# Performance work log

Hardware: AMD Instinct MI355X
Metric: run time of the kernel (lower is better)

## Reference

```python
import jax, jax.numpy as jnp
import numpy as np

WS = (7, 7, 7)          # (Wz, Wh, Ww)
NUM_HEADS = 3


def rel_position_index(ws):
    # Faithful to meshgrid_3d in the source: arrays are reversed, grid i varies
    # along axis i, so coords are stacked in (w, h, z) order.
    wz, wh, ww = ws
    g = np.meshgrid(np.arange(ww), np.arange(wh), np.arange(wz), indexing='ij')
    coords = np.stack(g)                      # (3, ww, wh, wz)
    flat = coords.reshape(3, -1)              # (3, N)
    rel = flat[:, :, None] - flat[:, None, :]  # (3, N, N)
    rel = rel.transpose(1, 2, 0).astype(np.int64)  # (N, N, 3)
    rel[:, :, 0] += wz - 1
    rel[:, :, 1] += wh - 1
    rel[:, :, 2] += ww - 1
    rel[:, :, 0] *= (2 * wh - 1) * (2 * ww - 1)
    rel[:, :, 1] *= (2 * ww - 1)
    return rel.sum(-1)                        # (N, N) in [0, (2W-1)^3)


REL_IDX = jnp.asarray(rel_position_index(WS).reshape(-1), dtype=jnp.int32)


def setup_inputs() -> dict:
    key = jax.random.key(0)
    ks = jax.random.split(key, 6)
    B, N, C = 256, 343, 96
    nW = 32
    x = jax.random.normal(ks[0], (B, N, C), dtype=jnp.float32)
    # shifted-window mask: 0 where attendable, -100 where blocked
    keep = jax.random.uniform(ks[1], (nW, N, N)) < 0.9
    mask = jnp.where(keep, 0.0, -100.0).astype(jnp.float32)
    w_qkv = jax.random.normal(ks[2], (C, 3 * C), dtype=jnp.float32) * 0.05
    b_qkv = jnp.zeros((3 * C,), jnp.float32)
    bias_table = jax.random.normal(ks[3], (2197, NUM_HEADS), dtype=jnp.float32) * 0.02
    w_proj = jax.random.normal(ks[4], (C, C), dtype=jnp.float32) * 0.05
    b_proj = jnp.zeros((C,), jnp.float32)
    return {"x": x, "mask": mask, "w_qkv": w_qkv, "b_qkv": b_qkv,
            "bias_table": bias_table, "w_proj": w_proj, "b_proj": b_proj}


def reference(x, mask, w_qkv, b_qkv, bias_table, w_proj, b_proj):
    B, N, C = x.shape
    H = NUM_HEADS
    hd = C // H
    scale = hd ** -0.5  # qk_scale is None -> head_dim**-0.5 (swin v1 path)
    # QKV projection, split to heads: (3, B, H, N, hd)
    qkv = (x @ w_qkv + b_qkv).reshape(B, N, 3, H, hd).transpose(2, 0, 3, 1, 4)
    q, k, v = qkv[0] * scale, qkv[1], qkv[2]
    attn = jnp.einsum('bhnd,bhmd->bhnm', q, k)        # (B, H, N, N)
    # gathered relative-position bias -> (H, N, N)
    bias = bias_table[REL_IDX].reshape(N, N, H).transpose(2, 0, 1)
    attn = attn + bias[None]
    # shifted-window mask add: reshape to (B//nW, nW, H, N, N)
    nW = mask.shape[0]
    attn = attn.reshape(B // nW, nW, H, N, N) + mask[None, :, None]
    attn = jax.nn.softmax(attn.reshape(B, H, N, N), axis=-1)
    out = jnp.einsum('bhnm,bhmd->bhnd', attn, v)      # (B, H, N, hd)
    out = out.transpose(0, 2, 1, 3).reshape(B, N, C)
    return out @ w_proj + b_proj
```

## Files before the change

kernel.cpp:

```cpp
#include <hip/hip_runtime.h>

#define N_TOK 343
#define NP 352
#define C_DIM 96
#define HEADS 3
#define HD 32
#define B_SZ 256
#define NW 32
#define QKV_COLS 288

#define QKV_ELEMS (B_SZ * HEADS * N_TOK * HD)
#define X2_ELEMS ((long)B_SZ * N_TOK * C_DIM)
#define CMB_ELEMS ((long)NW * HEADS * N_TOK * NP)

typedef _Float16 f16;
typedef _Float16 f16x2 __attribute__((ext_vector_type(2)));
typedef _Float16 f16x4 __attribute__((ext_vector_type(4)));
typedef _Float16 f16x8 __attribute__((ext_vector_type(8)));
typedef float f32x4 __attribute__((ext_vector_type(4)));

__global__ __launch_bounds__(256) void wprep_kernel(
    const float* __restrict__ w_qkv, const float* __restrict__ w_proj,
    f16* __restrict__ wt_qkv, f16* __restrict__ wt_proj) {
  const int e = blockIdx.x * 256 + threadIdx.x;
  if (e < QKV_COLS * 96) {
    const int cc = e / 96, k = e % 96;
    wt_qkv[e] = (f16)w_qkv[k * QKV_COLS + cc];
  } else {
    const int e2 = e - QKV_COLS * 96;
    if (e2 < 96 * 96) {
      const int cc = e2 / 96, k = e2 % 96;
      wt_proj[e2] = (f16)w_proj[k * 96 + cc];
    }
  }
}

__global__ __launch_bounds__(256) void cmb_kernel(
    const float* __restrict__ mask, const float* __restrict__ bias_table,
    f16* __restrict__ cmb) {
  const long e = (long)blockIdx.x * 256 + threadIdx.x;
  if (e >= CMB_ELEMS) return;
  const int key = (int)(e % NP);
  const long rowid = e / NP;
  const int q = (int)(rowid % N_TOK);
  const int wh = (int)(rowid / N_TOK);
  const int h = wh % HEADS;
  const int w = wh / HEADS;
  float val;
  if (key < N_TOK) {
    const int bn = (q / 49) * 169 + ((q / 7) % 7) * 13 + (q % 7);
    const int bm = (key / 49) * 169 + ((key / 7) % 7) * 13 + (key % 7);
    val = bias_table[(bn - bm + 1098) * HEADS + h] +
          mask[((long)w * N_TOK + q) * N_TOK + key];
  } else {
    val = -1000.f;
  }
  cmb[e] = (f16)val;
}

__global__ __launch_bounds__(256) void qkv_mfma_kernel(
    const float* __restrict__ x, const f16* __restrict__ wt,
    const float* __restrict__ bias,
    f16* __restrict__ Q, f16* __restrict__ K, f16* __restrict__ V) {
  __shared__ f16 sh[4][16][40];
  const int tid = threadIdx.x;
  const int wave = tid >> 6, lane = tid & 63;
  const int c = lane & 15, g = lane >> 4;
  const long rowTile = (long)blockIdx.x * 64 + wave * 16;
  const long arow = rowTile + c;

  f16x8 af[3];
#pragma unroll
  for (int ks = 0; ks < 3; ++ks) {
    const float* px = x + arow * 96 + ks * 32 + g * 8;
    const float4 lo = *(const float4*)px;
    const float4 hi = *(const float4*)(px + 4);
    f16x8 v;
    v[0] = (f16)lo.x; v[1] = (f16)lo.y; v[2] = (f16)lo.z; v[3] = (f16)lo.w;
    v[4] = (f16)hi.x; v[5] = (f16)hi.y; v[6] = (f16)hi.z; v[7] = (f16)hi.w;
    af[ks] = v;
  }

  const int rowL = (int)rowTile + (lane >> 2);
  const int bL = rowL / N_TOK, nL = rowL % N_TOK;

  const f32x4 zero = {0.f, 0.f, 0.f, 0.f};
  const float scale = 0.17677669529663687f;

#pragma unroll
  for (int p = 0; p < 9; ++p) {
    const int which = p / 3;
    const int h = p % 3;
    const float mult = (which == 0) ? scale : 1.0f;
#pragma unroll
    for (int e = 0; e < 2; ++e) {
      const int ct = 2 * p + e;
      f32x4 acc = zero;
#pragma unroll
      for (int ks = 0; ks < 3; ++ks) {
        const f16x8 bf = *(const f16x8*)(wt + (ct * 16 + c) * 96 + ks * 32 + g * 8);
        acc = __builtin_amdgcn_mfma_f32_16x16x32_f16(af[ks], bf, acc, 0, 0, 0);
      }
      const float bv = bias[ct * 16 + c];
#pragma unroll
      for (int r = 0; r < 4; ++r)
        sh[wave][4 * g + r][(e << 4) + c] = (f16)((acc[r] + bv) * mult);
    }
    __builtin_amdgcn_wave_barrier();
    const f16x8 po = *(const f16x8*)&sh[wave][lane >> 2][(lane & 3) * 8];
    __builtin_amdgcn_wave_barrier();
    f16* dst = (which == 0) ? Q : (which == 1) ? K : V;
    *(f16x8*)(dst + (((long)bL * HEADS + h) * N_TOK + nL) * HD + (lane & 3) * 8) = po;
  }
}

__global__ __launch_bounds__(512) void attn_kernel(
    const f16* __restrict__ Qh, const f16* __restrict__ Kh,
    const f16* __restrict__ Vh, const f16* __restrict__ CMB,
    f16* __restrict__ X2h) {
  __shared__ f16 Ks[NP][40];
  __shared__ f16 Vt[HD][356];

  const int blk = blockIdx.x;
  const int b = blk / HEADS;
  const int h = blk % HEADS;
  const int tid = threadIdx.x;
  const int wave = tid >> 6;
  const int lane = tid & 63;
  const int c = lane & 15;
  const int g = lane >> 4;

  const f16* Kg = Kh + (long)blk * (N_TOK * HD);
  const f16* Vg = Vh + (long)blk * (N_TOK * HD);
  const f16* Qg = Qh + (long)blk * (N_TOK * HD);

  for (int u = tid; u < NP * 4; u += 512) {
    const int key = u >> 2, j = u & 3;
    f16x8 val = {0, 0, 0, 0, 0, 0, 0, 0};
    if (key < N_TOK) val = *(const f16x8*)(Kg + key * HD + j * 8);
    *(f16x8*)&Ks[key][j * 8] = val;
  }
  for (int i = tid; i < N_TOK * 16; i += 512) {
    const int n = i >> 4, dp = i & 15;
    const f16x2 v2 = *(const f16x2*)(Vg + n * HD + dp * 2);
    Vt[2 * dp][n] = v2.x;
    Vt[2 * dp + 1][n] = v2.y;
  }
  for (int i = tid; i < HD * 13; i += 512) Vt[i / 13][N_TOK + i % 13] = (f16)0;
  __syncthreads();

  const int w = b & (NW - 1);
  const f32x4 zero = {0.f, 0.f, 0.f, 0.f};

  for (int qt = wave; qt < NP / 16; qt += 8) {
    const int q = qt * 16 + c;
    const int qrow = (q < N_TOK) ? q : (N_TOK - 1);
    const f16x8 qf = *(const f16x8*)(Qg + qrow * HD + g * 8);
    const f16* cmrow = CMB + ((long)(w * HEADS + h) * N_TOK + qrow) * NP;

    f32x4 acc0 = zero, acc1 = zero;
    float lsum = 0.f;

    for (int kt = 0; kt < NP / 32; ++kt) {
      const f16x8 kf0 = *(const f16x8*)&Ks[32 * kt + c][g * 8];
      const f16x8 kf1 = *(const f16x8*)&Ks[32 * kt + 16 + c][g * 8];
      const f16x4 cm0 = *(const f16x4*)(cmrow + 32 * kt + 4 * g);
      const f16x4 cm1 = *(const f16x4*)(cmrow + 32 * kt + 16 + 4 * g);

      const f32x4 s0 = __builtin_amdgcn_mfma_f32_16x16x32_f16(kf0, qf, zero, 0, 0, 0);
      const f32x4 s1 = __builtin_amdgcn_mfma_f32_16x16x32_f16(kf1, qf, zero, 0, 0, 0);

      float p0[4], p1[4];
#pragma unroll
      for (int r = 0; r < 4; ++r) {
        p0[r] = __expf(s0[r] + (float)cm0[r]);
        p1[r] = __expf(s1[r] + (float)cm1[r]);
        lsum += p0[r] + p1[r];
      }
      const f16x2 a0 = __builtin_bit_cast(f16x2, __builtin_amdgcn_cvt_pkrtz(p0[0], p0[1]));
      const f16x2 a1 = __builtin_bit_cast(f16x2, __builtin_amdgcn_cvt_pkrtz(p0[2], p0[3]));
      const f16x2 a2 = __builtin_bit_cast(f16x2, __builtin_amdgcn_cvt_pkrtz(p1[0], p1[1]));
      const f16x2 a3 = __builtin_bit_cast(f16x2, __builtin_amdgcn_cvt_pkrtz(p1[2], p1[3]));
      const f16x4 plo = __builtin_shufflevector(a0, a1, 0, 1, 2, 3);
      const f16x4 phi = __builtin_shufflevector(a2, a3, 0, 1, 2, 3);
      const f16x8 pf = __builtin_shufflevector(plo, phi, 0, 1, 2, 3, 4, 5, 6, 7);

      const f16x4 va0 = *(const f16x4*)&Vt[c][32 * kt + 4 * g];
      const f16x4 va1 = *(const f16x4*)&Vt[c][32 * kt + 16 + 4 * g];
      const f16x4 vb0 = *(const f16x4*)&Vt[16 + c][32 * kt + 4 * g];
      const f16x4 vb1 = *(const f16x4*)&Vt[16 + c][32 * kt + 16 + 4 * g];
      const f16x8 vf0 = __builtin_shufflevector(va0, va1, 0, 1, 2, 3, 4, 5, 6, 7);
      const f16x8 vf1 = __builtin_shufflevector(vb0, vb1, 0, 1, 2, 3, 4, 5, 6, 7);

      acc0 = __builtin_amdgcn_mfma_f32_16x16x32_f16(vf0, pf, acc0, 0, 0, 0);
      acc1 = __builtin_amdgcn_mfma_f32_16x16x32_f16(vf1, pf, acc1, 0, 0, 0);
    }

    lsum += __shfl_xor(lsum, 16);
    lsum += __shfl_xor(lsum, 32);
    const float inv = 1.f / lsum;

    if (q < N_TOK) {
      f16* orow = X2h + ((long)b * N_TOK + q) * C_DIM + h * HD;
      f16x4 o0, o1;
#pragma unroll
      for (int r = 0; r < 4; ++r) {
        o0[r] = (f16)(acc0[r] * inv);
        o1[r] = (f16)(acc1[r] * inv);
      }
      *(f16x4*)(orow + 4 * g) = o0;
      *(f16x4*)(orow + 16 + 4 * g) = o1;
    }
  }
}

__global__ __launch_bounds__(256) void proj_mfma_kernel(
    const f16* __restrict__ X2h, const f16* __restrict__ wt,
    const float* __restrict__ bias, float* __restrict__ out) {
  __shared__ float shp[4][16][100];
  const int tid = threadIdx.x;
  const int wave = tid >> 6, lane = tid & 63;
  const int c = lane & 15, g = lane >> 4;
  const long rowTile = (long)blockIdx.x * 64 + wave * 16;
  const long arow = rowTile + c;

  f16x8 af[3];
#pragma unroll
  for (int ks = 0; ks < 3; ++ks)
    af[ks] = *(const f16x8*)(X2h + arow * 96 + ks * 32 + g * 8);

  const f32x4 zero = {0.f, 0.f, 0.f, 0.f};
#pragma unroll
  for (int ct = 0; ct < 6; ++ct) {
    f32x4 acc = zero;
#pragma unroll
    for (int ks = 0; ks < 3; ++ks) {
      const f16x8 bf = *(const f16x8*)(wt + (ct * 16 + c) * 96 + ks * 32 + g * 8);
      acc = __builtin_amdgcn_mfma_f32_16x16x32_f16(af[ks], bf, acc, 0, 0, 0);
    }
    const float bv = bias[ct * 16 + c];
#pragma unroll
    for (int r = 0; r < 4; ++r)
      shp[wave][4 * g + r][ct * 16 + c] = acc[r] + bv;
  }
  __builtin_amdgcn_wave_barrier();
#pragma unroll
  for (int i = 0; i < 6; ++i) {
    const int u = lane + 64 * i;
    const int row = u / 24, ch = u % 24;
    const float4 v = *(const float4*)&shp[wave][row][ch * 4];
    *(float4*)(out + (rowTile + row) * 96 + ch * 4) = v;
  }
}

extern "C" void kernel_launch(void* const* d_in, const int* in_sizes, int n_in,
                              void* d_out, int out_size, void* d_ws, size_t ws_size,
                              hipStream_t stream) {
  const float* x          = (const float*)d_in[0];
  const float* mask       = (const float*)d_in[1];
  const float* w_qkv      = (const float*)d_in[2];
  const float* b_qkv      = (const float*)d_in[3];
  const float* bias_table = (const float*)d_in[4];
  const float* w_proj     = (const float*)d_in[5];
  const float* b_proj     = (const float*)d_in[6];
  float* out = (float*)d_out;

  f16* Qh = (f16*)d_ws;
  f16* Kh = Qh + QKV_ELEMS;
  f16* Vh = Kh + QKV_ELEMS;
  f16* X2h = Vh + QKV_ELEMS;
  f16* CMB = X2h + X2_ELEMS;
  f16* WTQ = CMB + CMB_ELEMS;
  f16* WTP = WTQ + QKV_COLS * 96;

  const int cmbBlocks = (int)((CMB_ELEMS + 255) / 256);
  const int wBlocks = (QKV_COLS * 96 + 96 * 96 + 255) / 256;
  const int gemmBlocks = (B_SZ * N_TOK) / 64;

  wprep_kernel<<<wBlocks, 256, 0, stream>>>(w_qkv, w_proj, WTQ, WTP);
  cmb_kernel<<<cmbBlocks, 256, 0, stream>>>(mask, bias_table, CMB);
  qkv_mfma_kernel<<<gemmBlocks, 256, 0, stream>>>(x, WTQ, b_qkv, Qh, Kh, Vh);
  attn_kernel<<<B_SZ * HEADS, 512, 0, stream>>>(Qh, Kh, Vh, CMB, X2h);
  proj_mfma_kernel<<<gemmBlocks, 256, 0, stream>>>(X2h, WTP, b_proj, out);
}
```

Before: 210.5 us.

## Use exp2 with log2e prescaling, restructure mask prep, prefetch mask, shrink attn blocks

Folds log2(e) into the Q scale and the combined bias/mask table so softmax can use the native exp2 instruction instead of __expf. The bias/mask prep kernel is reorganised to one block per (query, window), computing the gather index and mask load once and writing all three heads. The attention loop software-prefetches the next mask tile into registers, and the attention kernel drops from 512 to 256 threads per block with each wave covering more query tiles. Together these aim to cut transcendental cost, redundant prep work and global-load latency, at the cost of less parallelism per block and more registers held live.

```diff
diff --git a/kernel.cpp b/kernel.cpp
--- a/kernel.cpp
+++ b/kernel.cpp
@@ -35,27 +35,28 @@
   }
 }
 
-__global__ __launch_bounds__(256) void cmb_kernel(
+__global__ __launch_bounds__(384) void cmb_kernel(
     const float* __restrict__ mask, const float* __restrict__ bias_table,
     f16* __restrict__ cmb) {
-  const long e = (long)blockIdx.x * 256 + threadIdx.x;
-  if (e >= CMB_ELEMS) return;
-  const int key = (int)(e % NP);
-  const long rowid = e / NP;
-  const int q = (int)(rowid % N_TOK);
-  const int wh = (int)(rowid / N_TOK);
-  const int h = wh % HEADS;
-  const int w = wh / HEADS;
-  float val;
-  if (key < N_TOK) {
-    const int bn = (q / 49) * 169 + ((q / 7) % 7) * 13 + (q % 7);
+  const int q = blockIdx.x;
+  const int w = blockIdx.y;
+  const int key = threadIdx.x;
+  if (key >= NP) return;
+  const int bn = (q / 49) * 169 + ((q / 7) % 7) * 13 + (q % 7);
+  const float LOG2E = 1.4426950408889634f;
+  float mv = 0.f;
+  int idx = 0;
+  const bool valid = (key < N_TOK);
+  if (valid) {
     const int bm = (key / 49) * 169 + ((key / 7) % 7) * 13 + (key % 7);
-    val = bias_table[(bn - bm + 1098) * HEADS + h] +
-          mask[((long)w * N_TOK + q) * N_TOK + key];
-  } else {
-    val = -1000.f;
-  }
-  cmb[e] = (f16)val;
+    idx = (bn - bm + 1098) * HEADS;
+    mv = mask[((long)w * N_TOK + q) * N_TOK + key];
+  }
+#pragma unroll
+  for (int h = 0; h < HEADS; ++h) {
+    const float val = valid ? (bias_table[idx + h] + mv) * LOG2E : -14427.0f;
+    cmb[((long)(w * HEADS + h) * N_TOK + q) * NP + key] = (f16)val;
+  }
 }
 
 __global__ __launch_bounds__(256) void qkv_mfma_kernel(
@@ -85,7 +86,7 @@
   const int bL = rowL / N_TOK, nL = rowL % N_TOK;
 
   const f32x4 zero = {0.f, 0.f, 0.f, 0.f};
-  const float scale = 0.17677669529663687f;
+  const float scale = 0.17677669529663687f * 1.4426950408889634f;
 
 #pragma unroll
   for (int p = 0; p < 9; ++p) {
@@ -114,7 +115,7 @@
   }
 }
 
-__global__ __launch_bounds__(512) void attn_kernel(
+__global__ __launch_bounds__(256) void attn_kernel(
     const f16* __restrict__ Qh, const f16* __restrict__ Kh,
     const f16* __restrict__ Vh, const f16* __restrict__ CMB,
     f16* __restrict__ X2h) {
@@ -134,25 +135,25 @@
   const f16* Vg = Vh + (long)blk * (N_TOK * HD);
   const f16* Qg = Qh + (long)blk * (N_TOK * HD);
 
-  for (int u = tid; u < NP * 4; u += 512) {
+  for (int u = tid; u < NP * 4; u += 256) {
     const int key = u >> 2, j = u & 3;
     f16x8 val = {0, 0, 0, 0, 0, 0, 0, 0};
     if (key < N_TOK) val = *(const f16x8*)(Kg + key * HD + j * 8);
     *(f16x8*)&Ks[key][j * 8] = val;
   }
-  for (int i = tid; i < N_TOK * 16; i += 512) {
+  for (int i = tid; i < N_TOK * 16; i += 256) {
     const int n = i >> 4, dp = i & 15;
     const f16x2 v2 = *(const f16x2*)(Vg + n * HD + dp * 2);
     Vt[2 * dp][n] = v2.x;
     Vt[2 * dp + 1][n] = v2.y;
   }
-  for (int i = tid; i < HD * 13; i += 512) Vt[i / 13][N_TOK + i % 13] = (f16)0;
+  for (int i = tid; i < HD * 13; i += 256) Vt[i / 13][N_TOK + i % 13] = (f16)0;
   __syncthreads();
 
   const int w = b & (NW - 1);
   const f32x4 zero = {0.f, 0.f, 0.f, 0.f};
 
-  for (int qt = wave; qt < NP / 16; qt += 8) {
+  for (int qt = wave; qt < NP / 16; qt += 4) {
     const int q = qt * 16 + c;
     const int qrow = (q < N_TOK) ? q : (N_TOK - 1);
     const f16x8 qf = *(const f16x8*)(Qg + qrow * HD + g * 8);
@@ -161,11 +162,17 @@
     f32x4 acc0 = zero, acc1 = zero;
     float lsum = 0.f;
 
+    f16x4 cm0 = *(const f16x4*)(cmrow + 4 * g);
+    f16x4 cm1 = *(const f16x4*)(cmrow + 16 + 4 * g);
+
     for (int kt = 0; kt < NP / 32; ++kt) {
+      f16x4 ncm0, ncm1;
+      if (kt < NP / 32 - 1) {
+        ncm0 = *(const f16x4*)(cmrow + 32 * (kt + 1) + 4 * g);
+        ncm1 = *(const f16x4*)(cmrow + 32 * (kt + 1) + 16 + 4 * g);
+      }
       const f16x8 kf0 = *(const f16x8*)&Ks[32 * kt + c][g * 8];
       const f16x8 kf1 = *(const f16x8*)&Ks[32 * kt + 16 + c][g * 8];
-      const f16x4 cm0 = *(const f16x4*)(cmrow + 32 * kt + 4 * g);
-      const f16x4 cm1 = *(const f16x4*)(cmrow + 32 * kt + 16 + 4 * g);
 
       const f32x4 s0 = __builtin_amdgcn_mfma_f32_16x16x32_f16(kf0, qf, zero, 0, 0, 0);
       const f32x4 s1 = __builtin_amdgcn_mfma_f32_16x16x32_f16(kf1, qf, zero, 0, 0, 0);
@@ -173,8 +180,8 @@
       float p0[4], p1[4];
 #pragma unroll
       for (int r = 0; r < 4; ++r) {
-        p0[r] = __expf(s0[r] + (float)cm0[r]);
-        p1[r] = __expf(s1[r] + (float)cm1[r]);
+        p0[r] = __builtin_amdgcn_exp2f(s0[r] + (float)cm0[r]);
+        p1[r] = __builtin_amdgcn_exp2f(s1[r] + (float)cm1[r]);
         lsum += p0[r] + p1[r];
       }
       const f16x2 a0 = __builtin_bit_cast(f16x2, __builtin_amdgcn_cvt_pkrtz(p0[0], p0[1]));
@@ -194,6 +201,9 @@
 
       acc0 = __builtin_amdgcn_mfma_f32_16x16x32_f16(vf0, pf, acc0, 0, 0, 0);
       acc1 = __builtin_amdgcn_mfma_f32_16x16x32_f16(vf1, pf, acc1, 0, 0, 0);
+
+      cm0 = ncm0;
+      cm1 = ncm1;
     }
 
     lsum += __shfl_xor(lsum, 16);
@@ -273,13 +283,12 @@
   f16* WTQ = CMB + CMB_ELEMS;
   f16* WTP = WTQ + QKV_COLS * 96;
 
-  const int cmbBlocks = (int)((CMB_ELEMS + 255) / 256);
   const int wBlocks = (QKV_COLS * 96 + 96 * 96 + 255) / 256;
   const int gemmBlocks = (B_SZ * N_TOK) / 64;
 
   wprep_kernel<<<wBlocks, 256, 0, stream>>>(w_qkv, w_proj, WTQ, WTP);
-  cmb_kernel<<<cmbBlocks, 256, 0, stream>>>(mask, bias_table, CMB);
+  cmb_kernel<<<dim3(N_TOK, NW), 384, 0, stream>>>(mask, bias_table, CMB);
   qkv_mfma_kernel<<<gemmBlocks, 256, 0, stream>>>(x, WTQ, b_qkv, Qh, Kh, Vh);
-  attn_kernel<<<B_SZ * HEADS, 512, 0, stream>>>(Qh, Kh, Vh, CMB, X2h);
+  attn_kernel<<<B_SZ * HEADS, 256, 0, stream>>>(Qh, Kh, Vh, CMB, X2h);
   proj_mfma_kernel<<<gemmBlocks, 256, 0, stream>>>(X2h, WTP, b_proj, out);
 }
```

After: 200.6 us. 1.05x faster.
